# Optimization experiments

Hardware: AMD Instinct MI355X
Metric: run time of the kernel (lower is better)

Reference implementation:

```python
import jax, jax.numpy as jnp
import numpy as np

# delta_rule mode: order=1, gate_type='k', linear=True, trick='derivative' (n=1 expansion is identity)
B, H, S, D = 1, 16, 4096, 64
CHUNK = 64  # max_chunk_size, divides S
EPS = 1e-6


def setup_inputs() -> dict:
    key = jax.random.key(0)
    kq, kk, kv, kb = jax.random.split(key, 4)
    return {
        "q": jax.random.normal(kq, (B, H, S, D), jnp.float32),
        "k": jax.random.normal(kk, (B, H, S, D), jnp.float32),
        "v": jax.random.normal(kv, (B, H, S, D), jnp.float32),
        "beta": jax.random.uniform(kb, (B, H, S), jnp.float32),
    }


def _ensure_stability(x, lo=-10000.0, hi=10000.0):
    c = (hi + lo) / 2
    x = jnp.clip(x, lo, hi)
    return jnp.nan_to_num(x, nan=c, posinf=hi, neginf=lo)


def _l2norm(x):
    return x / (jnp.linalg.norm(x, axis=-1, keepdims=True) + EPS)


def _forward(q, k, v, beta):
    Bq, Hq, Sq, Dq = q.shape
    C = CHUNK
    Nc = Sq // C
    q = _l2norm(q)
    k = _l2norm(k)
    # gate_type 'k': clamp(beta, 1e-6, 1-1e-6)
    g = jnp.clip(beta, EPS, 1.0 - EPS)[..., None]
    k_beta = k * g
    v_beta = v * g
    ch = lambda x: x.reshape(Bq, Hq, Nc, C, Dq)  # chunk_sequence
    qc, kc, kbc, vbc = map(ch, (q, k, k_beta, v_beta))

    # UT transform: attn = -(k_beta k^T) strictly lower; T = (I - attn)^{-1}
    # fast_invert_matrix (forward substitution) == unit-lower triangular solve
    attn = -jnp.einsum('bhnid,bhnjd->bhnij', kbc, kc)
    strict = jnp.tril(jnp.ones((C, C), bool), k=-1)
    attn = jnp.where(strict, attn, 0.0)
    eye = jnp.eye(C, dtype=q.dtype)
    Tm = jax.lax.linalg.triangular_solve(
        eye - attn, jnp.broadcast_to(eye, attn.shape),
        left_side=True, lower=True, unit_diagonal=True)
    W = jnp.einsum('bhnij,bhnjd->bhnid', Tm, kbc)
    U = jnp.einsum('bhnij,bhnjd->bhnid', Tm, vbc)

    # sequential_delta_product_scan, n_orders=1: per-token state == broadcast h0
    def step(h0, xs):
        q_c, w_c, u_c = xs  # each [B,H,C,D]; h0 [B,H,D,D]
        kth = jnp.einsum('bhcd,bhde->bhce', w_c, h0)      # w_s @ h_old per token
        u_val = u_c - kth
        o_inter = jnp.einsum('bhcd,bhde->bhce', q_c, h0)  # q_s @ h_old
        o_intra = q_c * u_val                              # elementwise, as in source
        # per-token Householder state update; only last token's state propagates (n_orders=1)
        h_new = h0 + w_c[:, :, -1, :, None] * u_val[:, :, -1, None, :]
        h_new = _ensure_stability(h_new)
        return h_new, o_intra + o_inter

    xs = (jnp.moveaxis(qc, 2, 0), jnp.moveaxis(W, 2, 0), jnp.moveaxis(U, 2, 0))
    h0 = jnp.zeros((Bq, Hq, Dq, Dq), q.dtype)
    _, outs = jax.lax.scan(step, h0, xs)  # [Nc, B, H, C, D]
    return jnp.moveaxis(outs, 0, 2).reshape(Bq, Hq, Sq, Dq)


def reference(q, k, v, beta):
    return _forward(q, k, v, beta)
```

## Files before the change

### kernel.cpp

```cpp
#include <hip/hip_runtime.h>
#include <math.h>

#define BHn 16
#define SLEN 4096
#define Dd 64
#define Cc 64
#define NCC 64
#define EPSF 1e-6f
#define PD 65

__global__ __launch_bounds__(256, 4) void kA(
    const float* __restrict__ kg, const float* __restrict__ vg,
    const float* __restrict__ betag, float* __restrict__ WTg, float* __restrict__ UTg,
    float* __restrict__ wlast, float* __restrict__ ulast)
{
    const int n = blockIdx.x, bh = blockIdx.y, tid = threadIdx.x;
    __shared__ float KT[64 * PD];
    __shared__ float SM[64 * PD];
    __shared__ float gl[64];

    const size_t base = ((size_t)bh * SLEN + (size_t)n * Cc) * Dd;

    if (tid < 64) {
        const float b = betag[(size_t)bh * SLEN + n * Cc + tid];
        gl[tid] = fminf(fmaxf(b, EPSF), 1.0f - EPSF);
    }
#pragma unroll
    for (int p = 0; p < 4; p++) {
        const int flat = p * 1024 + tid * 4;
        const int row = flat >> 6, d0 = flat & 63;
        const float4 a = *(const float4*)(kg + base + flat);
        float ss = a.x * a.x + a.y * a.y + a.z * a.z + a.w * a.w;
        ss += __shfl_xor(ss, 1); ss += __shfl_xor(ss, 2);
        ss += __shfl_xor(ss, 4); ss += __shfl_xor(ss, 8);
        const float inv = 1.0f / (sqrtf(ss) + EPSF);
        KT[(d0 + 0) * PD + row] = a.x * inv;
        KT[(d0 + 1) * PD + row] = a.y * inv;
        KT[(d0 + 2) * PD + row] = a.z * inv;
        KT[(d0 + 3) * PD + row] = a.w * inv;
    }
    __syncthreads();

    float sol[64];
    if (tid < 64) {
#pragma unroll
        for (int j4 = 0; j4 < 16; j4++) {
            const float4 t4 = *(const float4*)&KT[tid * PD + j4 * 4];
            sol[j4 * 4 + 0] = t4.x * gl[j4 * 4 + 0];
            sol[j4 * 4 + 1] = t4.y * gl[j4 * 4 + 1];
            sol[j4 * 4 + 2] = t4.z * gl[j4 * 4 + 2];
            sol[j4 * 4 + 3] = t4.w * gl[j4 * 4 + 3];
        }
    } else if (tid < 200) {
        const int t = tid - 64;
        int ti = (int)((sqrtf(8.0f * (float)t + 1.0f) - 1.0f) * 0.5f);
        while (ti * (ti + 1) / 2 > t) --ti;
        while ((ti + 1) * (ti + 2) / 2 <= t) ++ti;
        const int tj = t - ti * (ti + 1) / 2;
        const int i0 = ti * 4, j0 = tj * 4;
        float sa[4][4];
#pragma unroll
        for (int r = 0; r < 4; r++)
#pragma unroll
            for (int c2 = 0; c2 < 4; c2++) sa[r][c2] = 0.f;
        for (int d = 0; d < 64; d++) {
            const float4 a = *(const float4*)&KT[d * PD + i0];
            const float4 b = *(const float4*)&KT[d * PD + j0];
            const float av[4] = {a.x, a.y, a.z, a.w};
            const float bv[4] = {b.x, b.y, b.z, b.w};
#pragma unroll
            for (int r = 0; r < 4; r++)
#pragma unroll
                for (int c2 = 0; c2 < 4; c2++) sa[r][c2] += av[r] * bv[c2];
        }
#pragma unroll
        for (int r = 0; r < 4; r++) {
            const float gg = gl[i0 + r];
            *(float4*)&SM[(i0 + r) * PD + j0] =
                make_float4(sa[r][0] * gg, sa[r][1] * gg, sa[r][2] * gg, sa[r][3] * gg);
        }
    }
    __syncthreads();

#pragma unroll
    for (int p = 0; p < 4; p++) {
        const int flat = p * 1024 + tid * 4;
        const int row = flat >> 6, d0 = flat & 63;
        const float4 a = *(const float4*)(vg + base + flat);
        const float gg = gl[row];
        KT[(d0 + 0) * PD + row] = a.x * gg;
        KT[(d0 + 1) * PD + row] = a.y * gg;
        KT[(d0 + 2) * PD + row] = a.z * gg;
        KT[(d0 + 3) * PD + row] = a.w * gg;
    }
    __syncthreads();

    if (tid >= 128 && tid < 192) {
        const int c = tid - 128;
#pragma unroll
        for (int j4 = 0; j4 < 16; j4++) {
            const float4 t4 = *(const float4*)&KT[c * PD + j4 * 4];
            sol[j4 * 4 + 0] = t4.x; sol[j4 * 4 + 1] = t4.y;
            sol[j4 * 4 + 2] = t4.z; sol[j4 * 4 + 3] = t4.w;
        }
    }
    if (tid < 64 || (tid >= 128 && tid < 192)) {
        const int c = tid & 63;
#pragma unroll
        for (int b = 0; b < 8; b++) {
            const int i0 = b * 8;
            float acc[8];
#pragma unroll
            for (int r = 0; r < 8; r++) acc[r] = sol[i0 + r];
#pragma unroll
            for (int j4 = 0; j4 < 2 * b; j4++) {
                const int j = j4 * 4;
                const float s0 = sol[j + 0], s1 = sol[j + 1];
                const float s2 = sol[j + 2], s3 = sol[j + 3];
#pragma unroll
                for (int r = 0; r < 8; r++) {
                    const float4 m4 = *(const float4*)&SM[(i0 + r) * PD + j];
                    acc[r] -= m4.x * s0 + m4.y * s1 + m4.z * s2 + m4.w * s3;
                }
            }
#pragma unroll
            for (int il = 1; il < 8; il++)
#pragma unroll
                for (int jl = 0; jl < il; jl++)
                    acc[il] -= SM[(i0 + il) * PD + i0 + jl] * acc[jl];
#pragma unroll
            for (int r = 0; r < 8; r++) sol[i0 + r] = acc[r];
        }
        float* dst = (tid < 64 ? WTg : UTg) +
                     (size_t)(bh * NCC + n) * Cc * Dd + (size_t)c * 64;
#pragma unroll
        for (int j4 = 0; j4 < 16; j4++)
            *(float4*)(dst + j4 * 4) = make_float4(sol[j4 * 4 + 0], sol[j4 * 4 + 1],
                                                   sol[j4 * 4 + 2], sol[j4 * 4 + 3]);
        float* lst = (tid < 64 ? wlast : ulast);
        lst[(size_t)(bh * NCC + n) * 64 + c] = sol[63];
    }
}

__global__ __launch_bounds__(256) void kB(
    const float* __restrict__ wlast, const float* __restrict__ ulast,
    float* __restrict__ Uvg)
{
    const int bh = blockIdx.x, tid = threadIdx.x;
    __shared__ float WL[64 * PD];
    __shared__ float UL[64 * PD];
    __shared__ float SM[64 * PD];
    const size_t gbase = (size_t)bh * NCC * 64;

#pragma unroll
    for (int p = 0; p < 4; p++) {
        const int flat = p * 1024 + tid * 4;
        const int m = flat >> 6, d = flat & 63;
        *(float4*)&WL[m * PD + d] = *(const float4*)(wlast + gbase + flat);
        *(float4*)&UL[m * PD + d] = *(const float4*)(ulast + gbase + flat);
    }
    __syncthreads();

    if (tid < 136) {
        int ti = (int)((sqrtf(8.0f * (float)tid + 1.0f) - 1.0f) * 0.5f);
        while (ti * (ti + 1) / 2 > tid) --ti;
        while ((ti + 1) * (ti + 2) / 2 <= tid) ++ti;
        const int tj = tid - ti * (ti + 1) / 2;
        const int i0 = ti * 4, j0 = tj * 4;
        float sa[4][4];
#pragma unroll
        for (int r = 0; r < 4; r++)
#pragma unroll
            for (int c2 = 0; c2 < 4; c2++) sa[r][c2] = 0.f;
        for (int d4 = 0; d4 < 16; d4++) {
            const int d = d4 * 4;
            float4 ar[4], bc[4];
#pragma unroll
            for (int r = 0; r < 4; r++) ar[r] = *(const float4*)&WL[(i0 + r) * PD + d];
#pragma unroll
            for (int c2 = 0; c2 < 4; c2++) bc[c2] = *(const float4*)&WL[(j0 + c2) * PD + d];
#pragma unroll
            for (int r = 0; r < 4; r++)
#pragma unroll
                for (int c2 = 0; c2 < 4; c2++)
                    sa[r][c2] += ar[r].x * bc[c2].x + ar[r].y * bc[c2].y +
                                 ar[r].z * bc[c2].z + ar[r].w * bc[c2].w;
        }
#pragma unroll
        for (int r = 0; r < 4; r++)
            *(float4*)&SM[(i0 + r) * PD + j0] =
                make_float4(sa[r][0], sa[r][1], sa[r][2], sa[r][3]);
    }
    __syncthreads();

    if (tid < 64) {
        const int e = tid;
        float sol[64];
#pragma unroll
        for (int m = 0; m < 64; m++) sol[m] = UL[m * PD + e];
#pragma unroll
        for (int b = 0; b < 8; b++) {
            const int i0 = b * 8;
            float acc[8];
#pragma unroll
            for (int r = 0; r < 8; r++) acc[r] = sol[i0 + r];
#pragma unroll
            for (int j4 = 0; j4 < 2 * b; j4++) {
                const int j = j4 * 4;
                const float s0 = sol[j + 0], s1 = sol[j + 1];
                const float s2 = sol[j + 2], s3 = sol[j + 3];
#pragma unroll
                for (int r = 0; r < 8; r++) {
                    const float4 m4 = *(const float4*)&SM[(i0 + r) * PD + j];
                    acc[r] -= m4.x * s0 + m4.y * s1 + m4.z * s2 + m4.w * s3;
                }
            }
#pragma unroll
            for (int il = 1; il < 8; il++)
#pragma unroll
                for (int jl = 0; jl < il; jl++)
                    acc[il] -= SM[(i0 + il) * PD + i0 + jl] * acc[jl];
#pragma unroll
            for (int r = 0; r < 8; r++) sol[i0 + r] = acc[r];
        }
#pragma unroll
        for (int m = 0; m < 64; m++) Uvg[gbase + (size_t)m * 64 + e] = sol[m];
    }
}

__global__ __launch_bounds__(256, 3) void kC(
    const float* __restrict__ qg, const float* __restrict__ WTg,
    const float* __restrict__ UTg, const float* __restrict__ wlast,
    const float* __restrict__ Uvg, float* __restrict__ outg)
{
    const int px = blockIdx.x, bh = blockIdx.y, tid = threadIdx.x;
    __shared__ float X1[64 * 64];
    __shared__ float X2[64 * PD];
    __shared__ float HB[64 * 64];
    const size_t lbase = (size_t)bh * NCC * 64;
    const int t0 = (tid >> 4) * 4, e0 = (tid & 15) * 4;

    for (int pass = 0; pass < 2; ++pass) {
        const int n = pass ? px : 63 - px;
        const size_t qbase = ((size_t)bh * SLEN + (size_t)n * Cc) * Dd;
        const size_t wbase = (size_t)(bh * NCC + n) * Cc * Dd;
        if (pass) __syncthreads();

        float4 qa[4], wt[4];
        float qinv[4];
#pragma unroll
        for (int p = 0; p < 4; p++) {
            const int flat = p * 1024 + tid * 4;
            const int m = flat >> 6, d = flat & 63;
            *(float4*)&X1[m * 64 + d] = *(const float4*)(wlast + lbase + flat);
            *(float4*)&X2[m * PD + d] = *(const float4*)(Uvg + lbase + flat);
            qa[p] = *(const float4*)(qg + qbase + flat);
            float ss = qa[p].x * qa[p].x + qa[p].y * qa[p].y +
                       qa[p].z * qa[p].z + qa[p].w * qa[p].w;
            ss += __shfl_xor(ss, 1); ss += __shfl_xor(ss, 2);
            ss += __shfl_xor(ss, 4); ss += __shfl_xor(ss, 8);
            qinv[p] = 1.0f / (sqrtf(ss) + EPSF);
            wt[p] = *(const float4*)(WTg + wbase + flat);
        }
        __syncthreads();

        float ha[4][4];
#pragma unroll
        for (int r = 0; r < 4; r++)
#pragma unroll
            for (int c2 = 0; c2 < 4; c2++) ha[r][c2] = 0.f;
        for (int m = 0; m < n; m++) {
            const float4 a = *(const float4*)&X1[m * 64 + t0];
            const float4 b = *(const float4*)&X2[m * PD + e0];
            const float av[4] = {a.x, a.y, a.z, a.w};
            const float bv[4] = {b.x, b.y, b.z, b.w};
#pragma unroll
            for (int r = 0; r < 4; r++)
#pragma unroll
                for (int c2 = 0; c2 < 4; c2++) ha[r][c2] += av[r] * bv[c2];
        }
#pragma unroll
        for (int r = 0; r < 4; r++)
            *(float4*)&HB[(t0 + r) * 64 + e0] =
                make_float4(ha[r][0], ha[r][1], ha[r][2], ha[r][3]);
        __syncthreads();

#pragma unroll
        for (int p = 0; p < 4; p++) {
            const int flat = p * 1024 + tid * 4;
            const int d = flat >> 6, t = flat & 63;
            *(float4*)&X1[d * 64 + t] = wt[p];
            const int row = d, d0 = t;
            X2[(d0 + 0) * PD + row] = qa[p].x * qinv[p];
            X2[(d0 + 1) * PD + row] = qa[p].y * qinv[p];
            X2[(d0 + 2) * PD + row] = qa[p].z * qinv[p];
            X2[(d0 + 3) * PD + row] = qa[p].w * qinv[p];
        }
        __syncthreads();

        float kth[4][4], oin[4][4];
#pragma unroll
        for (int r = 0; r < 4; r++)
#pragma unroll
            for (int c2 = 0; c2 < 4; c2++) { kth[r][c2] = 0.f; oin[r][c2] = 0.f; }
#pragma unroll 4
        for (int d = 0; d < 64; d++) {
            const float4 wv = *(const float4*)&X1[d * 64 + t0];
            const float4 qv = *(const float4*)&X2[d * PD + t0];
            const float4 hv = *(const float4*)&HB[d * 64 + e0];
            const float wa[4] = {wv.x, wv.y, wv.z, wv.w};
            const float qa2[4] = {qv.x, qv.y, qv.z, qv.w};
            const float hv4[4] = {hv.x, hv.y, hv.z, hv.w};
#pragma unroll
            for (int r = 0; r < 4; r++)
#pragma unroll
                for (int c2 = 0; c2 < 4; c2++) {
                    kth[r][c2] += wa[r] * hv4[c2];
                    oin[r][c2] += qa2[r] * hv4[c2];
                }
        }

        float* oc = outg + qbase;
        float o4[4][4];
#pragma unroll
        for (int s = 0; s < 4; s++) {
            const float4 u4 = *(const float4*)(UTg + wbase + (size_t)(e0 + s) * 64 + t0);
            const float4 q4 = *(const float4*)&X2[(e0 + s) * PD + t0];
            o4[0][s] = q4.x * (u4.x - kth[0][s]) + oin[0][s];
            o4[1][s] = q4.y * (u4.y - kth[1][s]) + oin[1][s];
            o4[2][s] = q4.z * (u4.z - kth[2][s]) + oin[2][s];
            o4[3][s] = q4.w * (u4.w - kth[3][s]) + oin[3][s];
        }
#pragma unroll
        for (int r = 0; r < 4; r++)
            *(float4*)(oc + (size_t)(t0 + r) * 64 + e0) =
                make_float4(o4[r][0], o4[r][1], o4[r][2], o4[r][3]);
    }
}

extern "C" void kernel_launch(void* const* d_in, const int* in_sizes, int n_in,
                              void* d_out, int out_size, void* d_ws, size_t ws_size,
                              hipStream_t stream) {
    const float* q    = (const float*)d_in[0];
    const float* k    = (const float*)d_in[1];
    const float* v    = (const float*)d_in[2];
    const float* beta = (const float*)d_in[3];
    float* out = (float*)d_out;

    float* WTg   = (float*)d_ws;
    float* UTg   = WTg + (size_t)BHn * NCC * Cc * Dd;
    float* wlast = UTg + (size_t)BHn * NCC * Cc * Dd;
    float* ulast = wlast + (size_t)BHn * NCC * 64;
    float* Uvg   = ulast + (size_t)BHn * NCC * 64;

    kA<<<dim3(NCC, BHn), 256, 0, stream>>>(k, v, beta, WTg, UTg, wlast, ulast);
    kB<<<dim3(BHn), 256, 0, stream>>>(wlast, ulast, Uvg);
    kC<<<dim3(32, BHn), 256, 0, stream>>>(q, WTg, UTg, wlast, Uvg, out);
}
```

Baseline: 84.07 us.

## Split kC output columns across two blocks and swizzle transposed q tile

kC now launches twice as many blocks, and each block computes only half of the 64 output value columns (32 each). The per-thread tile shrinks from 4x4 to 4x2. The transposed normalized-q tile is stored with an XOR swizzle instead of padding, and the state/Uv buffer is halved, which lowers LDS use and allows launch bounds of 4 blocks per CU. This adds parallelism and occupancy for a small grid (512 → 1024 blocks), at the cost of redundant q/W loads and normalization work in both halves.

```diff
diff --git a/kernel.cpp b/kernel.cpp
--- a/kernel.cpp
+++ b/kernel.cpp
@@ -228,17 +228,18 @@
     }
 }
 
-__global__ __launch_bounds__(256, 3) void kC(
+__global__ __launch_bounds__(256, 4) void kC(
     const float* __restrict__ qg, const float* __restrict__ WTg,
     const float* __restrict__ UTg, const float* __restrict__ wlast,
     const float* __restrict__ Uvg, float* __restrict__ outg)
 {
-    const int px = blockIdx.x, bh = blockIdx.y, tid = threadIdx.x;
-    __shared__ float X1[64 * 64];
-    __shared__ float X2[64 * PD];
-    __shared__ float HB[64 * 64];
+    const int bx = blockIdx.x, bh = blockIdx.y, tid = threadIdx.x;
+    const int px = bx >> 1, h = bx & 1;
+    __shared__ float X1[4096];
+    __shared__ float X2s[4096];
+    __shared__ float HBU[2048];
     const size_t lbase = (size_t)bh * NCC * 64;
-    const int t0 = (tid >> 4) * 4, e0 = (tid & 15) * 4;
+    const int t0 = (tid >> 4) * 4, e0 = (tid & 15) * 2;
 
     for (int pass = 0; pass < 2; ++pass) {
         const int n = pass ? px : 63 - px;
@@ -246,95 +247,99 @@
         const size_t wbase = (size_t)(bh * NCC + n) * Cc * Dd;
         if (pass) __syncthreads();
 
-        float4 qa[4], wt[4];
-        float qinv[4];
+        float4 wt[4];
 #pragma unroll
         for (int p = 0; p < 4; p++) {
             const int flat = p * 1024 + tid * 4;
-            const int m = flat >> 6, d = flat & 63;
-            *(float4*)&X1[m * 64 + d] = *(const float4*)(wlast + lbase + flat);
-            *(float4*)&X2[m * PD + d] = *(const float4*)(Uvg + lbase + flat);
-            qa[p] = *(const float4*)(qg + qbase + flat);
-            float ss = qa[p].x * qa[p].x + qa[p].y * qa[p].y +
-                       qa[p].z * qa[p].z + qa[p].w * qa[p].w;
+            const int row = flat >> 6, d0 = flat & 63;
+            *(float4*)&X1[row * 64 + d0] = *(const float4*)(wlast + lbase + flat);
+            wt[p] = *(const float4*)(WTg + wbase + flat);
+            const float4 qa = *(const float4*)(qg + qbase + flat);
+            float ss = qa.x * qa.x + qa.y * qa.y + qa.z * qa.z + qa.w * qa.w;
             ss += __shfl_xor(ss, 1); ss += __shfl_xor(ss, 2);
             ss += __shfl_xor(ss, 4); ss += __shfl_xor(ss, 8);
-            qinv[p] = 1.0f / (sqrtf(ss) + EPSF);
-            wt[p] = *(const float4*)(WTg + wbase + flat);
+            const float qinv = 1.0f / (sqrtf(ss) + EPSF);
+            const int cs = row ^ (((d0 >> 3) & 7) << 2);
+            X2s[(d0 + 0) * 64 + cs] = qa.x * qinv;
+            X2s[(d0 + 1) * 64 + cs] = qa.y * qinv;
+            X2s[(d0 + 2) * 64 + cs] = qa.z * qinv;
+            X2s[(d0 + 3) * 64 + cs] = qa.w * qinv;
+        }
+#pragma unroll
+        for (int p2 = 0; p2 < 2; p2++) {
+            const int flat = p2 * 1024 + tid * 4;
+            const int m = flat >> 5, e = flat & 31;
+            *(float4*)&HBU[m * 32 + e] =
+                *(const float4*)(Uvg + lbase + (size_t)m * 64 + h * 32 + e);
         }
         __syncthreads();
 
-        float ha[4][4];
-#pragma unroll
-        for (int r = 0; r < 4; r++)
-#pragma unroll
-            for (int c2 = 0; c2 < 4; c2++) ha[r][c2] = 0.f;
+        float ha[4][2];
+#pragma unroll
+        for (int r = 0; r < 4; r++) { ha[r][0] = 0.f; ha[r][1] = 0.f; }
         for (int m = 0; m < n; m++) {
             const float4 a = *(const float4*)&X1[m * 64 + t0];
-            const float4 b = *(const float4*)&X2[m * PD + e0];
-            const float av[4] = {a.x, a.y, a.z, a.w};
-            const float bv[4] = {b.x, b.y, b.z, b.w};
-#pragma unroll
-            for (int r = 0; r < 4; r++)
-#pragma unroll
-                for (int c2 = 0; c2 < 4; c2++) ha[r][c2] += av[r] * bv[c2];
-        }
-#pragma unroll
-        for (int r = 0; r < 4; r++)
-            *(float4*)&HB[(t0 + r) * 64 + e0] =
-                make_float4(ha[r][0], ha[r][1], ha[r][2], ha[r][3]);
+            const float2 b = *(const float2*)&HBU[m * 32 + e0];
+            ha[0][0] += a.x * b.x; ha[0][1] += a.x * b.y;
+            ha[1][0] += a.y * b.x; ha[1][1] += a.y * b.y;
+            ha[2][0] += a.z * b.x; ha[2][1] += a.z * b.y;
+            ha[3][0] += a.w * b.x; ha[3][1] += a.w * b.y;
+        }
         __syncthreads();
 
+#pragma unroll
+        for (int r = 0; r < 4; r++) {
+            float2 hw; hw.x = ha[r][0]; hw.y = ha[r][1];
+            *(float2*)&HBU[(t0 + r) * 32 + e0] = hw;
+        }
 #pragma unroll
         for (int p = 0; p < 4; p++) {
             const int flat = p * 1024 + tid * 4;
             const int d = flat >> 6, t = flat & 63;
             *(float4*)&X1[d * 64 + t] = wt[p];
-            const int row = d, d0 = t;
-            X2[(d0 + 0) * PD + row] = qa[p].x * qinv[p];
-            X2[(d0 + 1) * PD + row] = qa[p].y * qinv[p];
-            X2[(d0 + 2) * PD + row] = qa[p].z * qinv[p];
-            X2[(d0 + 3) * PD + row] = qa[p].w * qinv[p];
         }
         __syncthreads();
 
-        float kth[4][4], oin[4][4];
-#pragma unroll
-        for (int r = 0; r < 4; r++)
-#pragma unroll
-            for (int c2 = 0; c2 < 4; c2++) { kth[r][c2] = 0.f; oin[r][c2] = 0.f; }
+        float kth[4][2], oin[4][2];
+#pragma unroll
+        for (int r = 0; r < 4; r++) {
+            kth[r][0] = 0.f; kth[r][1] = 0.f;
+            oin[r][0] = 0.f; oin[r][1] = 0.f;
+        }
 #pragma unroll 4
         for (int d = 0; d < 64; d++) {
+            const int sw = ((d >> 3) & 7) << 2;
             const float4 wv = *(const float4*)&X1[d * 64 + t0];
-            const float4 qv = *(const float4*)&X2[d * PD + t0];
-            const float4 hv = *(const float4*)&HB[d * 64 + e0];
-            const float wa[4] = {wv.x, wv.y, wv.z, wv.w};
-            const float qa2[4] = {qv.x, qv.y, qv.z, qv.w};
-            const float hv4[4] = {hv.x, hv.y, hv.z, hv.w};
-#pragma unroll
-            for (int r = 0; r < 4; r++)
-#pragma unroll
-                for (int c2 = 0; c2 < 4; c2++) {
-                    kth[r][c2] += wa[r] * hv4[c2];
-                    oin[r][c2] += qa2[r] * hv4[c2];
-                }
+            const float4 qv = *(const float4*)&X2s[d * 64 + (t0 ^ sw)];
+            const float2 hv = *(const float2*)&HBU[d * 32 + e0];
+            kth[0][0] += wv.x * hv.x; kth[0][1] += wv.x * hv.y;
+            kth[1][0] += wv.y * hv.x; kth[1][1] += wv.y * hv.y;
+            kth[2][0] += wv.z * hv.x; kth[2][1] += wv.z * hv.y;
+            kth[3][0] += wv.w * hv.x; kth[3][1] += wv.w * hv.y;
+            oin[0][0] += qv.x * hv.x; oin[0][1] += qv.x * hv.y;
+            oin[1][0] += qv.y * hv.x; oin[1][1] += qv.y * hv.y;
+            oin[2][0] += qv.z * hv.x; oin[2][1] += qv.z * hv.y;
+            oin[3][0] += qv.w * hv.x; oin[3][1] += qv.w * hv.y;
         }
 
         float* oc = outg + qbase;
-        float o4[4][4];
-#pragma unroll
-        for (int s = 0; s < 4; s++) {
-            const float4 u4 = *(const float4*)(UTg + wbase + (size_t)(e0 + s) * 64 + t0);
-            const float4 q4 = *(const float4*)&X2[(e0 + s) * PD + t0];
+        float o4[4][2];
+#pragma unroll
+        for (int s = 0; s < 2; s++) {
+            const int e = h * 32 + e0 + s;
+            const int swe = ((e >> 3) & 7) << 2;
+            const float4 u4 = *(const float4*)(UTg + wbase + (size_t)e * 64 + t0);
+            const float4 q4 = *(const float4*)&X2s[e * 64 + (t0 ^ swe)];
             o4[0][s] = q4.x * (u4.x - kth[0][s]) + oin[0][s];
             o4[1][s] = q4.y * (u4.y - kth[1][s]) + oin[1][s];
             o4[2][s] = q4.z * (u4.z - kth[2][s]) + oin[2][s];
             o4[3][s] = q4.w * (u4.w - kth[3][s]) + oin[3][s];
         }
 #pragma unroll
-        for (int r = 0; r < 4; r++)
-            *(float4*)(oc + (size_t)(t0 + r) * 64 + e0) =
-                make_float4(o4[r][0], o4[r][1], o4[r][2], o4[r][3]);
+        for (int r = 0; r < 4; r++) {
+            float2 ow; ow.x = o4[r][0]; ow.y = o4[r][1];
+            *(float2*)(oc + (size_t)(t0 + r) * 64 + h * 32 + e0) = ow;
+        }
     }
 }
 
@@ -355,5 +360,5 @@
 
     kA<<<dim3(NCC, BHn), 256, 0, stream>>>(k, v, beta, WTg, UTg, wlast, ulast);
     kB<<<dim3(BHn), 256, 0, stream>>>(wlast, ulast, Uvg);
-    kC<<<dim3(32, BHn), 256, 0, stream>>>(q, WTg, UTg, wlast, Uvg, out);
+    kC<<<dim3(64, BHn), 256, 0, stream>>>(q, WTg, UTg, wlast, Uvg, out);
 }
```

New measurement: 90.63 us. 7.8% more time.

## Pack strict-lower triangle into padded LDS and broadcast via readlane in solve

Applied to the files above, without the earlier changes.

The strictly-lower part of the 64x64 k_beta k^T matrix is now stored in kernel A as a packed triangle (2016 entries, padded every 32). Each lane of the solving wavefront loads 32 negated entries into registers. The forward substitution then takes each coefficient with __builtin_amdgcn_readlane, so the inner loop no longer reads the matrix from LDS. This removes repeated shared-memory traffic in the triangular solve, but the loop becomes fully unrolled over about 2016 steps, which grows code size and may increase register pressure.

```diff
diff --git a/kernel.cpp b/kernel.cpp
--- a/kernel.cpp
+++ b/kernel.cpp
@@ -16,7 +16,7 @@
 {
     const int n = blockIdx.x, bh = blockIdx.y, tid = threadIdx.x;
     __shared__ float KT[64 * PD];
-    __shared__ float SM[64 * PD];
+    __shared__ float SMf[2112];
     __shared__ float gl[64];
 
     const size_t base = ((size_t)bh * SLEN + (size_t)n * Cc) * Dd;
@@ -75,9 +75,16 @@
         }
 #pragma unroll
         for (int r = 0; r < 4; r++) {
-            const float gg = gl[i0 + r];
-            *(float4*)&SM[(i0 + r) * PD + j0] =
-                make_float4(sa[r][0] * gg, sa[r][1] * gg, sa[r][2] * gg, sa[r][3] * gg);
+            const int i = i0 + r;
+            const int eb = (i * (i - 1)) / 2 + j0;
+            const float gg = gl[i];
+#pragma unroll
+            for (int c2 = 0; c2 < 4; c2++) {
+                if (ti != tj || c2 < r) {
+                    const int e = eb + c2;
+                    SMf[e + (e >> 5)] = sa[r][c2] * gg;
+                }
+            }
         }
     }
     __syncthreads();
@@ -106,30 +113,25 @@
     }
     if (tid < 64 || (tid >= 128 && tid < 192)) {
         const int c = tid & 63;
-#pragma unroll
-        for (int b = 0; b < 8; b++) {
-            const int i0 = b * 8;
-            float acc[8];
-#pragma unroll
-            for (int r = 0; r < 8; r++) acc[r] = sol[i0 + r];
-#pragma unroll
-            for (int j4 = 0; j4 < 2 * b; j4++) {
-                const int j = j4 * 4;
-                const float s0 = sol[j + 0], s1 = sol[j + 1];
-                const float s2 = sol[j + 2], s3 = sol[j + 3];
-#pragma unroll
-                for (int r = 0; r < 8; r++) {
-                    const float4 m4 = *(const float4*)&SM[(i0 + r) * PD + j];
-                    acc[r] -= m4.x * s0 + m4.y * s1 + m4.z * s2 + m4.w * s3;
-                }
+        float sm[32];
+        {
+            const int lb = 33 * c;
+#pragma unroll
+            for (int r8 = 0; r8 < 8; r8++) {
+                const float4 t4 = *(const float4*)&SMf[lb + r8 * 4];
+                sm[r8 * 4 + 0] = -t4.x; sm[r8 * 4 + 1] = -t4.y;
+                sm[r8 * 4 + 2] = -t4.z; sm[r8 * 4 + 3] = -t4.w;
             }
-#pragma unroll
-            for (int il = 1; il < 8; il++)
-#pragma unroll
-                for (int jl = 0; jl < il; jl++)
-                    acc[il] -= SM[(i0 + il) * PD + i0 + jl] * acc[jl];
-#pragma unroll
-            for (int r = 0; r < 8; r++) sol[i0 + r] = acc[r];
+        }
+#pragma unroll
+        for (int j = 0; j < 63; j++) {
+#pragma unroll
+            for (int i = j + 1; i < 64; i++) {
+                const int e = (i * (i - 1)) / 2 + j;
+                const float s = __int_as_float(__builtin_amdgcn_readlane(
+                    __float_as_int(sm[e & 31]), e >> 5));
+                sol[i] += s * sol[j];
+            }
         }
         float* dst = (tid < 64 ? WTg : UTg) +
                      (size_t)(bh * NCC + n) * Cc * Dd + (size_t)c * 64;
```

After: 86.49 us. 1.03x slower.
